# Kernel tuning notes

Measured on AMD Instinct MI355X. Metric: run time of the kernel, lower is better.

The kernel has to match this reference:

```python
import jax, jax.numpy as jnp
import numpy as np

C_IN, C_OUT, K = 2048, 1024, 2  # k=2 -> 5x5 correlation window
B, H, W = 4, 64, 64


def conv1x1(x, w, b):
    # x: [B,C,H,W], w: [O,C], b: [O]
    return jnp.einsum('bchw,oc->bohw', x, w) + b[None, :, None, None]


def bn_star(x, Kstd=3.0):
    # torch.std is unbiased (ddof=1); clip outliers above mu+K*std to 1
    mu = jnp.mean(x, axis=0, keepdims=True)
    std = jnp.std(x, axis=0, ddof=1, keepdims=True)
    lim = mu + Kstd * std
    return jnp.where(x > lim, jnp.float32(1.0), x)


def match_trans(curr_F, prev_F, prev_M):
    # curr_F/prev_F: [B,2048,H,W]; prev_M: [B,1024,H,W]
    b, c, h, w = prev_F.shape
    prev_nc = jnp.sum(prev_F, axis=1)  # [B,H,W]
    curr_nc = jnp.sum(curr_F, axis=1)  # [B,H,W]
    pad_nc = jnp.pad(prev_nc, ((0, 0), (K, K), (K, K)))
    pad_M = jnp.pad(prev_M, ((0, 0), (0, 0), (K, K), (K, K)))
    # shifted copies: shift(i,j)(y,x) = prev_nc_padded(y-i, x-j)
    shifts = jnp.stack([pad_nc[:, K - i:K - i + h, K - j:K - j + w]
                        for i in range(-K, K + 1) for j in range(-K, K + 1)], axis=0)  # [25,B,H,W]
    # sum_filter(prev_F) summed over channels == C * 5x5 local sum of prev_nc
    denom = curr_nc * (jnp.float32(c) * jnp.sum(shifts, axis=0))  # [B,H,W]
    aligned = jnp.zeros_like(prev_M)
    idx = 0
    for i in range(-K, K + 1):
        for j in range(-K, K + 1):
            mask_ij = curr_nc * shifts[idx] / denom  # [B,H,W]
            aligned = aligned + mask_ij[:, None] * pad_M[:, :, K - i:K - i + h, K - j:K - j + w]
            idx += 1
    return aligned


def setup_inputs() -> dict:
    key = jax.random.key(0)
    ks = jax.random.split(key, 16)
    s = jnp.float32(0.02)
    inp = {
        'curr_F': jax.random.uniform(ks[0], (B, C_IN, H, W), jnp.float32),
        'prev_F': jax.random.uniform(ks[1], (B, C_IN, H, W), jnp.float32),
        'prev_M': jax.random.normal(ks[2], (B, C_OUT, H, W), jnp.float32),
        'Wz_w': jax.random.normal(ks[3], (C_OUT, C_IN), jnp.float32) * s,
        'Wz_b': jnp.zeros((C_OUT,), jnp.float32),
        'Wr_w': jax.random.normal(ks[4], (C_OUT, C_IN), jnp.float32) * s,
        'Wr_b': jnp.zeros((C_OUT,), jnp.float32),
        'W_w': jax.random.normal(ks[5], (C_OUT, C_IN), jnp.float32) * s,
        'W_b': jnp.zeros((C_OUT,), jnp.float32),
        'Uz_w': jax.random.normal(ks[6], (C_OUT, C_OUT), jnp.float32) * s,
        'Uz_b': jnp.zeros((C_OUT,), jnp.float32),
        'Ur_w': jax.random.normal(ks[7], (C_OUT, C_OUT), jnp.float32) * s,
        'Ur_b': jnp.zeros((C_OUT,), jnp.float32),
        'U_w': jax.random.normal(ks[8], (C_OUT, C_OUT), jnp.float32) * s,
        'U_b': jnp.zeros((C_OUT,), jnp.float32),
        'body': 1,
    }
    return inp


def reference(curr_F, prev_F, prev_M, Wz_w, Wz_b, Wr_w, Wr_b, W_w, W_b,
              Uz_w, Uz_b, Ur_w, Ur_b, U_w, U_b, body):
    if body:
        aligned = match_trans(curr_F, prev_F, prev_M)
    else:
        aligned = prev_M
    zt = bn_star(jax.nn.relu(conv1x1(curr_F, Wz_w, Wz_b) + conv1x1(aligned, Uz_w, Uz_b)))
    rt = bn_star(jax.nn.relu(conv1x1(curr_F, Wr_w, Wr_b) + conv1x1(aligned, Ur_w, Ur_b)))
    M = jax.nn.relu(conv1x1(curr_F, W_w, W_b) + conv1x1(aligned * rt, U_w, U_b))
    curr_M = (1.0 - zt) * aligned + zt * M
    return curr_M
```

## Files before the change

kernel.cpp:

```cpp
#include <hip/hip_runtime.h>
#include <hip/hip_bf16.h>

namespace {

constexpr int NB = 4;
constexpr int CI = 2048;
constexpr int CO = 1024;
constexpr int HW = 4096;
constexpr int MTOT = NB * HW;

typedef __attribute__((ext_vector_type(8))) short bf16x8;
typedef __attribute__((ext_vector_type(4))) float f32x4;
typedef __hip_bfloat16 bf16;

__device__ __forceinline__ void g2l16(void* lds, const void* g) {
  __builtin_amdgcn_global_load_lds((const __attribute__((address_space(1))) void*)g,
                                   (__attribute__((address_space(3))) void*)lds,
                                   16, 0, 0);
}

__global__ void zero_k(float* __restrict__ p, int n) {
  int i = blockIdx.x * 256 + threadIdx.x;
  if (i < n) p[i] = 0.f;
}

__global__ void castw6_k(const float* s0, const float* s1, const float* s2,
                         const float* s3, const float* s4, const float* s5,
                         bf16* d0, bf16* d1, bf16* d2, bf16* d3, bf16* d4, bf16* d5) {
  int y = blockIdx.y;
  const float* s = (y == 0) ? s0 : (y == 1) ? s1 : (y == 2) ? s2 : (y == 3) ? s3 : (y == 4) ? s4 : s5;
  bf16* d = (y == 0) ? d0 : (y == 1) ? d1 : (y == 2) ? d2 : (y == 3) ? d3 : (y == 4) ? d4 : d5;
  int n4 = ((y < 3) ? CI * CO : CO * CO) >> 2;
  int i = blockIdx.x * 256 + threadIdx.x;
  if (i < n4) {
    float4 v = ((const float4*)s)[i];
    union { ushort4 u; bf16 h[4]; } pk;
    pk.h[0] = __float2bfloat16(v.x);
    pk.h[1] = __float2bfloat16(v.y);
    pk.h[2] = __float2bfloat16(v.z);
    pk.h[3] = __float2bfloat16(v.w);
    ((ushort4*)d)[i] = pk.u;
  }
}

__global__ void nc_sum_k(const float* __restrict__ src, float* __restrict__ dst) {
  int p = blockIdx.x * 256 + threadIdx.x;
  int c0 = blockIdx.y * 128;
  int b = blockIdx.z;
  const float* s = src + ((long)b * CI + c0) * HW + p;
  float a = 0.f;
  #pragma unroll 8
  for (int c = 0; c < 128; ++c) a += s[(long)c * HW];
  atomicAdd(dst + b * HW + p, a);
}

template <typename TO>
__global__ void transpose64_k(const float* __restrict__ src, TO* __restrict__ dst,
                              int R, int S) {
  __shared__ float tile[64][65];
  const int b = blockIdx.z;
  const int r0 = blockIdx.x * 64, s0 = blockIdx.y * 64;
  const int t = threadIdx.x;
  const int fc = t & 15;
  const int rr = t >> 4;
  const float* sp = src + ((size_t)b * R + r0) * S + s0;
  #pragma unroll
  for (int i = 0; i < 4; ++i) {
    float4 v = *(const float4*)(sp + (size_t)(rr + i * 16) * S + fc * 4);
    tile[rr + i * 16][fc * 4 + 0] = v.x;
    tile[rr + i * 16][fc * 4 + 1] = v.y;
    tile[rr + i * 16][fc * 4 + 2] = v.z;
    tile[rr + i * 16][fc * 4 + 3] = v.w;
  }
  __syncthreads();
  #pragma unroll
  for (int i = 0; i < 4; ++i) {
    const int sr = rr + i * 16;
    float4 w;
    w.x = tile[fc * 4 + 0][sr];
    w.y = tile[fc * 4 + 1][sr];
    w.z = tile[fc * 4 + 2][sr];
    w.w = tile[fc * 4 + 3][sr];
    if constexpr (sizeof(TO) == 4) {
      *(float4*)((float*)dst + ((size_t)b * S + s0 + sr) * R + r0 + fc * 4) = w;
    } else {
      union { ushort4 u; bf16 h[4]; } pk;
      pk.h[0] = __float2bfloat16(w.x);
      pk.h[1] = __float2bfloat16(w.y);
      pk.h[2] = __float2bfloat16(w.z);
      pk.h[3] = __float2bfloat16(w.w);
      *(ushort4*)((bf16*)dst + ((size_t)b * S + s0 + sr) * R + r0 + fc * 4) = pk.u;
    }
  }
}

__global__ void boxinv_k(const float* __restrict__ nc, float* __restrict__ invden) {
  int i = blockIdx.x * 256 + threadIdx.x;
  int b = i >> 12, p = i & 4095;
  int y = p >> 6, x = p & 63;
  float s = 0.f;
  #pragma unroll
  for (int dy = -2; dy <= 2; ++dy) {
    int yy = y + dy;
    if ((unsigned)yy >= 64u) continue;
    #pragma unroll
    for (int dx = -2; dx <= 2; ++dx) {
      int xx = x + dx;
      if ((unsigned)xx >= 64u) continue;
      s += nc[b * HW + yy * 64 + xx];
    }
  }
  invden[i] = 1.f / (2048.f * s);
}

__global__ void align_k(const float* __restrict__ pmcl, const float* __restrict__ nc,
                        const float* __restrict__ invden, const int* __restrict__ body,
                        bf16* __restrict__ ah) {
  int bp = blockIdx.x;
  int b = bp >> 12, p = bp & 4095;
  int y = p >> 6, x = p & 63;
  int c = threadIdx.x * 4;
  float4 acc = make_float4(0.f, 0.f, 0.f, 0.f);
  if (body[0]) {
    #pragma unroll
    for (int dy = -2; dy <= 2; ++dy) {
      int yy = y + dy;
      if ((unsigned)yy >= 64u) continue;
      #pragma unroll
      for (int dx = -2; dx <= 2; ++dx) {
        int xx = x + dx;
        if ((unsigned)xx >= 64u) continue;
        int sp = yy * 64 + xx;
        float w = nc[b * HW + sp];
        float4 v = *(const float4*)(pmcl + ((long)b * HW + sp) * CO + c);
        acc.x += w * v.x; acc.y += w * v.y; acc.z += w * v.z; acc.w += w * v.w;
      }
    }
    float s = invden[bp];
    acc.x *= s; acc.y *= s; acc.z *= s; acc.w *= s;
  } else {
    acc = *(const float4*)(pmcl + (long)bp * CO + c);
  }
  union { ushort4 u; bf16 h[4]; } pk;
  pk.h[0] = __float2bfloat16(acc.x);
  pk.h[1] = __float2bfloat16(acc.y);
  pk.h[2] = __float2bfloat16(acc.z);
  pk.h[3] = __float2bfloat16(acc.w);
  *(ushort4*)(ah + (long)bp * CO + c) = pk.u;
}

template <int MODE>
__global__ __launch_bounds__(512, 2) void gemm256(
    const bf16* __restrict__ A1, const bf16* __restrict__ B1,
    const bf16* __restrict__ A2, const bf16* __restrict__ B2,
    const float* __restrict__ bias1, const float* __restrict__ bias2,
    const bf16* __restrict__ ztp, const bf16* __restrict__ aligh,
    bf16* __restrict__ outh, float* __restrict__ outcf) {
  constexpr int NT1 = CI / 32;
  constexpr int NT = NT1 + CO / 32;
  __shared__ __align__(16) char lds[131072];
  const int t = threadIdx.x, lane = t & 63, wid = t >> 6;
  const int wm = wid >> 2, wn = wid & 3;
  const int m0 = blockIdx.x * 256, n0 = blockIdx.y * 256;
  const int fr = lane & 15, kq = lane >> 4;

  const int b0i = (wid << 7) + lane;
  const int line0 = b0i >> 3;
  const int c3 = (b0i & 7) ^ (line0 & 7);
  const int row0 = 2 * line0 + (c3 >> 2);
  const int k16 = c3 & 3;
  const char* pa1 = (const char*)A1 + (((size_t)(m0 + row0) * CI + k16 * 8) << 1);
  const char* pa1h = pa1 + ((size_t)CI << 5);
  const char* pb1 = (const char*)B1 + (((size_t)(n0 + row0) * CI + k16 * 8) << 1);
  const char* pb1h = pb1 + ((size_t)CI << 5);
  const char* pa2 = (const char*)A2 + (((size_t)(m0 + row0) * CO + k16 * 8) << 1);
  const char* pa2h = pa2 + ((size_t)CO << 5);
  const char* pb2 = (const char*)B2 + (((size_t)(n0 + row0) * CO + k16 * 8) << 1);
  const char* pb2h = pb2 + ((size_t)CO << 5);

  auto STAGE = [&](int s) {
    const char *sa, *sah, *sb, *sbh;
    if (s < NT1) {
      size_t so = (size_t)s << 6;
      sa = pa1 + so; sah = pa1h + so; sb = pb1 + so; sbh = pb1h + so;
    } else {
      size_t so = (size_t)(s - NT1) << 6;
      sa = pa2 + so; sah = pa2h + so; sb = pb2 + so; sbh = pb2h + so;
    }
    char* d = lds + ((s & 3) << 15) + (wid << 11) + (lane << 4);
    g2l16(d, sa);
    g2l16(d + 1024, sah);
    g2l16(d + 16384, sb);
    g2l16(d + 17408, sbh);
  };

  int offA[8], offB[4];
  #pragma unroll
  for (int mi = 0; mi < 8; ++mi) {
    int r = (wm << 7) + (mi << 4) + fr;
    int ln = r >> 1;
    int cc = ((r & 1) << 2) | kq;
    offA[mi] = (ln << 7) + ((cc ^ (ln & 7)) << 4);
  }
  #pragma unroll
  for (int ni = 0; ni < 4; ++ni) {
    int r = (wn << 6) + (ni << 4) + fr;
    int ln = r >> 1;
    int cc = ((r & 1) << 2) | kq;
    offB[ni] = 16384 + (ln << 7) + ((cc ^ (ln & 7)) << 4);
  }

  f32x4 acc[8][4] = {};

  STAGE(0); STAGE(1);

  #pragma unroll 1
  for (int tp = 0; tp < NT; ++tp) {
    if (tp + 2 < NT) {
      STAGE(tp + 2);
      asm volatile("s_waitcnt vmcnt(8)" ::: "memory");
    } else if (tp + 1 < NT) {
      asm volatile("s_waitcnt vmcnt(4)" ::: "memory");
    } else {
      asm volatile("s_waitcnt vmcnt(0)" ::: "memory");
    }
    __builtin_amdgcn_s_barrier();
    asm volatile("" ::: "memory");
    const char* buf = lds + ((tp & 3) << 15);
    bf16x8 av[8], bv[4];
    #pragma unroll
    for (int mi = 0; mi < 8; ++mi) av[mi] = *(const bf16x8*)(buf + offA[mi]);
    #pragma unroll
    for (int ni = 0; ni < 4; ++ni) bv[ni] = *(const bf16x8*)(buf + offB[ni]);
    __builtin_amdgcn_s_setprio(1);
    #pragma unroll
    for (int mi = 0; mi < 8; ++mi)
      #pragma unroll
      for (int ni = 0; ni < 4; ++ni)
        acc[mi][ni] = __builtin_amdgcn_mfma_f32_16x16x32_bf16(av[mi], bv[ni], acc[mi][ni], 0, 0, 0);
    __builtin_amdgcn_s_setprio(0);
    asm volatile("" ::: "memory");
  }

  #pragma unroll
  for (int mi = 0; mi < 8; ++mi) {
    const int r0 = m0 + (wm << 7) + (mi << 4) + (kq << 2);
    #pragma unroll
    for (int ni = 0; ni < 4; ++ni) {
      const int col = n0 + (wn << 6) + (ni << 4) + fr;
      const float bsum = bias1[col] + bias2[col];
      if (MODE == 2) {
        const int bb = r0 >> 12, p0 = r0 & 4095;
        float4 o;
        float* po = &o.x;
        #pragma unroll
        for (int j = 0; j < 4; ++j) {
          const size_t idx = (size_t)(r0 + j) * CO + col;
          float m = fmaxf(acc[mi][ni][j] + bsum, 0.f);
          float z = __bfloat162float(ztp[idx]);
          float a = __bfloat162float(aligh[idx]);
          po[j] = (1.f - z) * a + z * m;
        }
        *(float4*)(outcf + ((size_t)bb * CO + col) * HW + p0) = o;
      } else {
        #pragma unroll
        for (int j = 0; j < 4; ++j) {
          const size_t idx = (size_t)(r0 + j) * CO + col;
          float v = acc[mi][ni][j] + bsum;
          if (MODE == 0) {
            outh[idx] = __float2bfloat16(fmaxf(v, 0.f));
          } else {
            float rt = fmaxf(v, 0.f);
            outh[idx] = __float2bfloat16(__bfloat162float(aligh[idx]) * rt);
          }
        }
      }
    }
  }
}

}

extern "C" void kernel_launch(void* const* d_in, const int* in_sizes, int n_in,
                              void* d_out, int out_size, void* d_ws, size_t ws_size,
                              hipStream_t stream) {
  const float* curr_F = (const float*)d_in[0];
  const float* prev_F = (const float*)d_in[1];
  const float* prev_M = (const float*)d_in[2];
  const float* Wz_w = (const float*)d_in[3];
  const float* Wz_b = (const float*)d_in[4];
  const float* Wr_w = (const float*)d_in[5];
  const float* Wr_b = (const float*)d_in[6];
  const float* W_w  = (const float*)d_in[7];
  const float* W_b  = (const float*)d_in[8];
  const float* Uz_w = (const float*)d_in[9];
  const float* Uz_b = (const float*)d_in[10];
  const float* Ur_w = (const float*)d_in[11];
  const float* Ur_b = (const float*)d_in[12];
  const float* U_w  = (const float*)d_in[13];
  const float* U_b  = (const float*)d_in[14];
  const int* body   = (const int*)d_in[15];
  float* out = (float*)d_out;

  char* ws = (char*)d_ws;
  const size_t M64 = 1ull << 26;
  const size_t M32 = 1ull << 25;
  bf16*  currF_h   = (bf16*)(ws);
  float* prevM_cl  = (float*)(ws + M64);
  bf16*  zt        = (bf16*)(ws + M64);
  bf16*  align_h   = (bf16*)(ws + 2 * M64);
  bf16*  ar_h      = (bf16*)(ws + 2 * M64 + M32);
  char*  wb        = ws + 2 * M64 + 2 * M32;
  bf16* Wz_h = (bf16*)wb;
  bf16* Wr_h = Wz_h + (size_t)CO * CI;
  bf16* W_h  = Wr_h + (size_t)CO * CI;
  bf16* Uz_h = W_h  + (size_t)CO * CI;
  bf16* Ur_h = Uz_h + (size_t)CO * CO;
  bf16* U_h  = Ur_h + (size_t)CO * CO;
  float* prev_nc = (float*)(U_h + (size_t)CO * CO);
  float* invden  = prev_nc + NB * HW;

  castw6_k<<<dim3((CI * CO) / 1024, 6), 256, 0, stream>>>(
      Wz_w, Wr_w, W_w, Uz_w, Ur_w, U_w, Wz_h, Wr_h, W_h, Uz_h, Ur_h, U_h);

  zero_k<<<dim3((NB * HW) / 256), 256, 0, stream>>>(prev_nc, NB * HW);
  nc_sum_k<<<dim3(HW / 256, CI / 128, NB), 256, 0, stream>>>(prev_F, prev_nc);

  transpose64_k<bf16><<<dim3(CI / 64, HW / 64, NB), 256, 0, stream>>>(curr_F, currF_h, CI, HW);
  transpose64_k<float><<<dim3(CO / 64, HW / 64, NB), 256, 0, stream>>>(prev_M, prevM_cl, CO, HW);

  boxinv_k<<<dim3((NB * HW) / 256), 256, 0, stream>>>(prev_nc, invden);
  align_k<<<dim3(NB * HW), 256, 0, stream>>>(prevM_cl, prev_nc, invden, body, align_h);

  dim3 gg(MTOT / 256, CO / 256);
  gemm256<0><<<gg, 512, 0, stream>>>(currF_h, Wz_h, align_h, Uz_h,
                                     Wz_b, Uz_b, nullptr, nullptr, zt, nullptr);
  gemm256<3><<<gg, 512, 0, stream>>>(currF_h, Wr_h, align_h, Ur_h,
                                     Wr_b, Ur_b, nullptr, align_h, ar_h, nullptr);
  gemm256<2><<<gg, 512, 0, stream>>>(currF_h, W_h, ar_h, U_h,
                                     W_b, U_b, zt, align_h, nullptr, out);
}
```

Baseline: 520.9 us.

## Double K tile to 64 with two-stage LDS buffering in fused GEMM

```diff
diff --git a/kernel.cpp b/kernel.cpp
--- a/kernel.cpp
+++ b/kernel.cpp
@@ -156,8 +156,8 @@
     const float* __restrict__ bias1, const float* __restrict__ bias2,
     const bf16* __restrict__ ztp, const bf16* __restrict__ aligh,
     bf16* __restrict__ outh, float* __restrict__ outcf) {
-  constexpr int NT1 = CI / 32;
-  constexpr int NT = NT1 + CO / 32;
+  constexpr int NT1 = CI / 64;
+  constexpr int NT = NT1 + CO / 64;
   __shared__ __align__(16) char lds[131072];
   const int t = threadIdx.x, lane = t & 63, wid = t >> 6;
   const int wm = wid >> 2, wn = wid & 3;
@@ -180,18 +180,23 @@
 
   auto STAGE = [&](int s) {
     const char *sa, *sah, *sb, *sbh;
+    size_t so;
     if (s < NT1) {
-      size_t so = (size_t)s << 6;
+      so = (size_t)s << 7;
       sa = pa1 + so; sah = pa1h + so; sb = pb1 + so; sbh = pb1h + so;
     } else {
-      size_t so = (size_t)(s - NT1) << 6;
+      so = (size_t)(s - NT1) << 7;
       sa = pa2 + so; sah = pa2h + so; sb = pb2 + so; sbh = pb2h + so;
     }
-    char* d = lds + ((s & 3) << 15) + (wid << 11) + (lane << 4);
+    char* d = lds + ((s & 1) << 16) + (wid << 11) + (lane << 4);
     g2l16(d, sa);
     g2l16(d + 1024, sah);
-    g2l16(d + 16384, sb);
-    g2l16(d + 17408, sbh);
+    g2l16(d + 16384, sa + 64);
+    g2l16(d + 17408, sah + 64);
+    g2l16(d + 32768, sb);
+    g2l16(d + 33792, sbh);
+    g2l16(d + 49152, sb + 64);
+    g2l16(d + 50176, sbh + 64);
   };
 
   int offA[8], offB[4];
@@ -207,31 +212,36 @@
     int r = (wn << 6) + (ni << 4) + fr;
     int ln = r >> 1;
     int cc = ((r & 1) << 2) | kq;
-    offB[ni] = 16384 + (ln << 7) + ((cc ^ (ln & 7)) << 4);
+    offB[ni] = 32768 + (ln << 7) + ((cc ^ (ln & 7)) << 4);
   }
 
   f32x4 acc[8][4] = {};
 
-  STAGE(0); STAGE(1);
+  STAGE(0);
 
   #pragma unroll 1
   for (int tp = 0; tp < NT; ++tp) {
-    if (tp + 2 < NT) {
-      STAGE(tp + 2);
-      asm volatile("s_waitcnt vmcnt(8)" ::: "memory");
-    } else if (tp + 1 < NT) {
-      asm volatile("s_waitcnt vmcnt(4)" ::: "memory");
-    } else {
-      asm volatile("s_waitcnt vmcnt(0)" ::: "memory");
-    }
+    asm volatile("s_waitcnt vmcnt(0)" ::: "memory");
     __builtin_amdgcn_s_barrier();
     asm volatile("" ::: "memory");
-    const char* buf = lds + ((tp & 3) << 15);
+    if (tp + 1 < NT) STAGE(tp + 1);
+    const char* buf = lds + ((tp & 1) << 16);
     bf16x8 av[8], bv[4];
     #pragma unroll
     for (int mi = 0; mi < 8; ++mi) av[mi] = *(const bf16x8*)(buf + offA[mi]);
     #pragma unroll
     for (int ni = 0; ni < 4; ++ni) bv[ni] = *(const bf16x8*)(buf + offB[ni]);
+    __builtin_amdgcn_s_setprio(1);
+    #pragma unroll
+    for (int mi = 0; mi < 8; ++mi)
+      #pragma unroll
+      for (int ni = 0; ni < 4; ++ni)
+        acc[mi][ni] = __builtin_amdgcn_mfma_f32_16x16x32_bf16(av[mi], bv[ni], acc[mi][ni], 0, 0, 0);
+    __builtin_amdgcn_s_setprio(0);
+    #pragma unroll
+    for (int mi = 0; mi < 8; ++mi) av[mi] = *(const bf16x8*)(buf + 16384 + offA[mi]);
+    #pragma unroll
+    for (int ni = 0; ni < 4; ++ni) bv[ni] = *(const bf16x8*)(buf + 16384 + offB[ni]);
     __builtin_amdgcn_s_setprio(1);
     #pragma unroll
     for (int mi = 0; mi < 8; ++mi)
```

After: 525.1 us. Within noise of the previous version (+0.8%).
